# Performance work log

Hardware: AMD Instinct MI355X
Metric: run time of the kernel (lower is better)

The kernel has to match this reference:

```python
import jax, jax.numpy as jnp
import numpy as np

N_ATOMS = 32768
N_GRAPHS = 256
PER_GRAPH = 128
HIDDEN = 128
FILTERS = 128
NUM_GAUSS = 50
CUTOFF = 5.0
NUM_LAYERS = 3
OUT_CH = 1
BOX = 14.1
SLOPE = 0.015


def _lrelu(x):
    return jnp.where(x > 0, x, SLOPE * x)


def setup_inputs() -> dict:
    rng = np.random.default_rng(0)
    batch = np.repeat(np.arange(N_GRAPHS), PER_GRAPH).astype(np.int64)
    pos_np = rng.uniform(0.0, BOX, size=(N_ATOMS, 3)).astype(np.float32)
    # radius graph, built per-graph exactly like compute_radius_graph
    # (with global index offset so edges reference global node ids)
    edges = []
    for b in range(N_GRAPHS):
        pb = pos_np[b * PER_GRAPH:(b + 1) * PER_GRAPH]
        d = np.linalg.norm(pb[:, None, :] - pb[None, :, :], axis=-1)
        src, dst = np.where((d <= CUTOFF) & (d > 0))
        edges.append(np.stack([src, dst], axis=0) + b * PER_GRAPH)
    edge_index = np.concatenate(edges, axis=1).astype(np.int64)
    z = rng.integers(0, 100, size=(N_ATOMS,)).astype(np.int64)

    key = jax.random.key(0)
    ks = jax.random.split(key, 12)

    def xavier(k, shape):
        fan_in, fan_out = shape[-2], shape[-1]
        s = float(np.sqrt(6.0 / (fan_in + fan_out)))
        return jax.random.uniform(k, shape, jnp.float32, -s, s)

    L = NUM_LAYERS
    params = dict(
        emb=jax.random.normal(ks[0], (100, HIDDEN), jnp.float32),
        w_lin=xavier(ks[1], (L, HIDDEN, FILTERS)),
        mlp_w1=xavier(ks[2], (L, NUM_GAUSS, FILTERS)), mlp_b1=jnp.zeros((L, FILTERS), jnp.float32),
        mlp_w2=xavier(ks[3], (L, FILTERS, FILTERS)), mlp_b2=jnp.zeros((L, FILTERS), jnp.float32),
        mlp_w3=xavier(ks[4], (L, FILTERS, FILTERS)), mlp_b3=jnp.zeros((L, FILTERS), jnp.float32),
        lout_w=xavier(ks[5], (L, FILTERS, FILTERS)), lout_b=jnp.zeros((L, FILTERS), jnp.float32),
        v_w1=xavier(ks[6], (L, FILTERS, HIDDEN)), v_b1=jnp.zeros((L, HIDDEN), jnp.float32),
        v_w2=xavier(ks[7], (L, HIDDEN, HIDDEN)), v_b2=jnp.zeros((L, HIDDEN), jnp.float32),
        u_w1=xavier(ks[8], (HIDDEN, HIDDEN // 2)), u_b1=jnp.zeros((HIDDEN // 2,), jnp.float32),
        u_w2=xavier(ks[9], (HIDDEN // 2, OUT_CH)), u_b2=jnp.zeros((OUT_CH,), jnp.float32),
    )
    return dict(z=jnp.asarray(z), pos=jnp.asarray(pos_np), batch=jnp.asarray(batch),
                edge_index=jnp.asarray(edge_index), **params)


def reference(z, pos, batch, edge_index, emb, w_lin,
              mlp_w1, mlp_b1, mlp_w2, mlp_b2, mlp_w3, mlp_b3,
              lout_w, lout_b, v_w1, v_b1, v_w2, v_b2,
              u_w1, u_b1, u_w2, u_b2):
    row, col = edge_index[0], edge_index[1]          # row = j (source), col = i (target)
    dist = jnp.linalg.norm(pos[row] - pos[col], axis=-1)        # [E]
    offset = jnp.linspace(0.0, CUTOFF, NUM_GAUSS)
    coeff = -0.5 / (offset[1] - offset[0]) ** 2
    dist_emb = jnp.exp(coeff * (dist[:, None] - offset[None, :]) ** 2)   # [E, G]
    C = 0.5 * (jnp.cos(dist * jnp.pi / CUTOFF) + 1.0)                    # [E]

    v = emb[z]                                                           # [N, H]
    for l in range(NUM_LAYERS):
        # UpdateE: filter MLP on distance embedding, cosine cutoff envelope
        h = _lrelu(dist_emb @ mlp_w1[l] + mlp_b1[l])
        h = _lrelu(h @ mlp_w2[l] + mlp_b2[l])
        W = (h @ mlp_w3[l] + mlp_b3[l]) * C[:, None]                     # [E, F]
        e = (v @ w_lin[l])[row] * W                                      # gather + modulate
        e = (e @ lout_w[l] + lout_b[l]) + e                              # residual edge lin
        # UpdateV: scatter-add into target nodes, then 2-layer MLP residual
        agg = jax.ops.segment_sum(e, col, num_segments=N_ATOMS)         # [N, F]
        v = v + (_lrelu(agg @ v_w1[l] + v_b1[l]) @ v_w2[l] + v_b2[l])

    # UpdateU: node MLP then per-graph mean pooling
    u = _lrelu(v @ u_w1 + u_b1) @ u_w2 + u_b2                            # [N, out]
    sums = jax.ops.segment_sum(u, batch, num_segments=N_GRAPHS)
    cnt = jax.ops.segment_sum(jnp.ones((u.shape[0],), u.dtype), batch, num_segments=N_GRAPHS)
    return jnp.where(cnt[:, None] > 0, sums / jnp.maximum(cnt, 1.0)[:, None], 0.0)
```

## Files before the change

kernel.cpp:

```cpp
#include <hip/hip_runtime.h>

typedef float f4 __attribute__((ext_vector_type(4)));
typedef float f2 __attribute__((ext_vector_type(2)));
typedef float f32x4 __attribute__((ext_vector_type(4)));
typedef short bf16x8 __attribute__((ext_vector_type(8)));
typedef short sh4 __attribute__((ext_vector_type(4)));

#define G_TAB 2048
#define SWZ(row, b) ((b) ^ (((row) & 7) << 4))

__device__ __forceinline__ float lrelu(float x) { return x > 0.f ? x : 0.015f * x; }

__device__ __forceinline__ short f2bf(float x) {
  union { float f; unsigned u; } v; v.f = x;
  unsigned r = v.u + 0x7fff + ((v.u >> 16) & 1);
  return (short)(r >> 16);
}
__device__ __forceinline__ float bf2f(short h) {
  union { float f; unsigned u; } v; v.u = ((unsigned)(unsigned short)h) << 16;
  return v.f;
}

__device__ __forceinline__ void st_pair(short* Hi, short* Lo, int row, int k, f4 x) {
  sh4 hi, lo;
  #pragma unroll
  for (int c = 0; c < 4; c++) { hi[c] = f2bf(x[c]); lo[c] = f2bf(x[c] - bf2f(hi[c])); }
  int b = row * 256 + SWZ(row, (k >> 3) * 16) + (k & 7) * 2;
  *(sh4*)((char*)Hi + b) = hi;
  *(sh4*)((char*)Lo + b) = lo;
}
__device__ __forceinline__ void st_pair1(short* Hi, short* Lo, int row, int k, float x) {
  short hi = f2bf(x), lo = f2bf(x - bf2f(hi));
  int b = row * 256 + SWZ(row, (k >> 3) * 16) + (k & 7) * 2;
  *(short*)((char*)Hi + b) = hi;
  *(short*)((char*)Lo + b) = lo;
}

template<int NFC, int CH>
__device__ __forceinline__ void mm16(const short* Ahi, const short* Alo,
    const short* __restrict__ BhT, const short* __restrict__ BlT,
    int w, int l, f32x4* acc) {
  int lr = l & 15, lk = l >> 4;
  #pragma unroll
  for (int fc = 0; fc < NFC; fc++) acc[fc] = (f32x4)0.f;
  #pragma unroll
  for (int ch = 0; ch < CH; ch++) {
    int arow = w * 16 + lr;
    int ab = arow * 256 + SWZ(arow, ch * 64 + lk * 16);
    bf16x8 ah = *(const bf16x8*)((const char*)Ahi + ab);
    bf16x8 al = *(const bf16x8*)((const char*)Alo + ab);
    #pragma unroll
    for (int fc = 0; fc < NFC; fc++) {
      int bcol = fc * 16 + lr;
      int bb = bcol * 256 + SWZ(bcol, ch * 64 + lk * 16);
      bf16x8 bh = *(const bf16x8*)((const char*)BhT + bb);
      bf16x8 bl = *(const bf16x8*)((const char*)BlT + bb);
      acc[fc] = __builtin_amdgcn_mfma_f32_16x16x32_bf16(ah, bh, acc[fc], 0, 0, 0);
      acc[fc] = __builtin_amdgcn_mfma_f32_16x16x32_bf16(al, bh, acc[fc], 0, 0, 0);
      acc[fc] = __builtin_amdgcn_mfma_f32_16x16x32_bf16(ah, bl, acc[fc], 0, 0, 0);
    }
  }
}


__global__ __launch_bounds__(256) void gather_emb(const int* __restrict__ z,
    const float* __restrict__ emb, float* __restrict__ v, int nf4) {
  int i = blockIdx.x * 256 + threadIdx.x;
  if (i >= nf4) return;
  int a = i >> 5, s = i & 31;
  ((f4*)v)[i] = ((const f4*)emb)[z[a] * 32 + s];
}

__global__ __launch_bounds__(256) void edge_geom(const int* __restrict__ ei,
    const float* __restrict__ pos, float* __restrict__ edc, int E) {
  int e = blockIdx.x * 256 + threadIdx.x;
  if (e >= E) return;
  int r = ei[e], c = ei[E + e];
  float dx = pos[3*r] - pos[3*c];
  float dy = pos[3*r+1] - pos[3*c+1];
  float dz = pos[3*r+2] - pos[3*c+2];
  float d = sqrtf(dx*dx + dy*dy + dz*dz);
  edc[2*e] = d;
  edc[2*e+1] = 0.5f * (cosf(d * 0.6283185307179586f) + 1.0f);
}

__global__ __launch_bounds__(256) void make_starts(const int* __restrict__ row,
    int* __restrict__ starts, int E, int N) {
  int i = blockIdx.x * 256 + threadIdx.x;
  if (i > N) return;
  int lo = 0, hi = E;
  while (lo < hi) { int mid = (lo + hi) >> 1; if (row[mid] < i) lo = mid + 1; else hi = mid; }
  starts[i] = lo;
}

__global__ __launch_bounds__(256) void convert_wt(const float* __restrict__ w_lin,
    const float* __restrict__ vw2, const float* __restrict__ uw1,
    const float* __restrict__ mw1, const float* __restrict__ mw2,
    const float* __restrict__ mw3, const float* __restrict__ vw1,
    short* __restrict__ dhi, short* __restrict__ dlo) {
  int y = blockIdx.y;
  int i = blockIdx.x * 256 + threadIdx.x;
  int j = i >> 7, k = i & 127;
  int slot; float x;
  if (y < 3)       { slot = y;     x = w_lin[(size_t)y*16384 + k*128 + j]; }
  else if (y < 6)  { slot = 3 + y; x = vw2[(size_t)(y-3)*16384 + k*128 + j]; }
  else if (y == 6) { slot = 9;     x = (j < 64) ? uw1[k*64 + j] : 0.f; }
  else if (y < 10) { slot = 3 + y; x = mw2[(size_t)(y-7)*16384 + k*128 + j]; }
  else if (y < 13) { slot = 3 + y; x = mw3[(size_t)(y-10)*16384 + k*128 + j]; }
  else if (y < 16) { slot = 3 + y; x = (k < 50) ? mw1[(size_t)(y-13)*6400 + k*128 + j] : 0.f; }
  else             { slot = 3 + y; x = vw1[(size_t)(y-16)*16384 + k*128 + j]; }
  short hi = f2bf(x);
  int ob = j * 256 + (((k >> 3) * 16) ^ ((j & 7) << 4)) + (k & 7) * 2;
  char* bh = (char*)dhi + (size_t)slot * 32768;
  char* bl = (char*)dlo + (size_t)slot * 32768;
  *(short*)(bh + ob) = hi;
  *(short*)(bl + ob) = f2bf(x - bf2f(hi));
}

__global__ __launch_bounds__(128) void make_c1(const float* __restrict__ lball,
    const float* __restrict__ w1all, float* __restrict__ c1all) {
  int l = blockIdx.y;
  const float* lb = lball + (size_t)l * 128;
  const float* w1 = w1all + (size_t)l * 16384;
  int j = threadIdx.x;
  float s = 0.f;
  for (int k = 0; k < 128; k++) s += lb[k] * w1[k * 128 + j];
  c1all[l * 128 + j] = s;
}

__global__ __launch_bounds__(512) void prep_M(const float* __restrict__ loutw,
    short* __restrict__ whiT, short* __restrict__ wloT) {
  __shared__ __align__(16) short Ahi[16384];
  __shared__ __align__(16) short Alo[16384];
  int tid = threadIdx.x;
  int lay = blockIdx.x;
  int w = tid >> 6, l = tid & 63;
  int lr = l & 15, lk = l >> 4;
  int arow = w * 16 + (l >> 2), sub = l & 3;
  const f4* src = (const f4*)(loutw + (size_t)lay*16384 + (size_t)arow*128 + sub*32);
  #pragma unroll
  for (int q = 0; q < 8; q++) {
    f4 x = src[q];
    int kb = sub * 32 + q * 4;
    #pragma unroll
    for (int cc = 0; cc < 4; cc++) if (arow == kb + cc) x[cc] += 1.0f;
    st_pair(Ahi, Alo, arow, kb, x);
  }
  __syncthreads();
  f32x4 acc[8];
  mm16<8,4>(Ahi, Alo, whiT + (size_t)(19+lay)*16384, wloT + (size_t)(19+lay)*16384, w, l, acc);
  char* bh = (char*)whiT + (size_t)(3+lay) * 32768;
  char* bl = (char*)wloT + (size_t)(3+lay) * 32768;
  #pragma unroll
  for (int r = 0; r < 4; r++)
    #pragma unroll
    for (int fc = 0; fc < 8; fc++) {
      int row = w*16 + lk*4 + r, col = fc*16 + lr;
      float val = acc[fc][r];
      short hi = f2bf(val);
      int ob = col * 256 + (((row >> 3) * 16) ^ ((col & 7) << 4)) + (row & 7) * 2;
      *(short*)(bh + ob) = hi;
      *(short*)(bl + ob) = f2bf(val - bf2f(hi));
    }
}

__global__ __launch_bounds__(512) void table_mfma(
    const short* __restrict__ whiT, const short* __restrict__ wloT,
    const float* __restrict__ mb1, const float* __restrict__ mb2,
    const float* __restrict__ mb3, float* __restrict__ tables) {
  __shared__ __align__(16) short Ahi[16384];
  __shared__ __align__(16) short Alo[16384];
  __shared__ __align__(16) short Bhi[16384];
  __shared__ __align__(16) short Blo[16384];
  int tid = threadIdx.x;
  int lay = blockIdx.y;
  int p0 = blockIdx.x * 128;
  int w = tid >> 6, l = tid & 63;
  int lr = l & 15, lk = l >> 4;
  int prow = w * 16 + (l >> 2), sub = l & 3;
  const float delta = 5.0f / (G_TAB - 1);
  {
    float d = (p0 + prow) * delta;
    #pragma unroll
    for (int q = 0; q < 4; q++) {
      f4 x;
      #pragma unroll
      for (int cc = 0; cc < 4; cc++) {
        int k = sub * 16 + q * 4 + cc;
        float t = d - k * (5.0f / 49.0f);
        x[cc] = (k < 50) ? expf(-48.02f * t * t) : 0.f;
      }
      st_pair(Ahi, Alo, prow, sub * 16 + q * 4, x);
    }
  }
  __syncthreads();
  f32x4 acc[8];
  mm16<8,2>(Ahi, Alo, whiT + (size_t)(16+lay)*16384, wloT + (size_t)(16+lay)*16384, w, l, acc);
  #pragma unroll
  for (int r = 0; r < 4; r++)
    #pragma unroll
    for (int fc = 0; fc < 8; fc++)
      st_pair1(Bhi, Blo, w*16 + lk*4 + r, fc*16 + lr,
               lrelu(acc[fc][r] + mb1[lay*128 + fc*16 + lr]));
  __syncthreads();
  mm16<8,4>(Bhi, Blo, whiT + (size_t)(10+lay)*16384, wloT + (size_t)(10+lay)*16384, w, l, acc);
  #pragma unroll
  for (int r = 0; r < 4; r++)
    #pragma unroll
    for (int fc = 0; fc < 8; fc++)
      st_pair1(Ahi, Alo, w*16 + lk*4 + r, fc*16 + lr,
               lrelu(acc[fc][r] + mb2[lay*128 + fc*16 + lr]));
  __syncthreads();
  mm16<8,4>(Ahi, Alo, whiT + (size_t)(13+lay)*16384, wloT + (size_t)(13+lay)*16384, w, l, acc);
  float* tb = tables + (size_t)lay * G_TAB * 128;
  #pragma unroll
  for (int r = 0; r < 4; r++)
    #pragma unroll
    for (int fc = 0; fc < 8; fc++)
      tb[(size_t)(p0 + w*16 + lk*4 + r) * 128 + fc*16 + lr] =
          acc[fc][r] + mb3[lay*128 + fc*16 + lr];
}


template<int ACT, int ACC, int BIAS>
__global__ __launch_bounds__(256) void gemm128b(
    const float* __restrict__ A, const short* __restrict__ BhS,
    const short* __restrict__ BlS, const float* __restrict__ bias,
    const float* __restrict__ bias2, const float* __restrict__ rs,
    float* __restrict__ out) {
  __shared__ __align__(16) short Bhi[16384];
  __shared__ __align__(16) short Blo[16384];
  int tid = threadIdx.x;
  int p = blockIdx.x;
  size_t row0 = (size_t)(((p & 7) << 5) + (p >> 3)) * 128;
  #pragma unroll
  for (int s = 0; s < 8; s++) {
    ((bf16x8*)Bhi)[tid + 256*s] = ((const bf16x8*)BhS)[tid + 256*s];
    ((bf16x8*)Blo)[tid + 256*s] = ((const bf16x8*)BlS)[tid + 256*s];
  }
  __syncthreads();
  int w = tid >> 6, l = tid & 63, lr = l & 15, lk = l >> 4;
  #pragma unroll
  for (int half = 0; half < 2; half++) {
    int rbase = half * 64 + w * 16;
    const float* ap0 = A + (row0 + rbase + lr) * 128;
    bf16x8 ah[4], al[4];
    #pragma unroll
    for (int ch = 0; ch < 4; ch++) {
      const f4* ap = (const f4*)(ap0 + ch*32 + lk*8);
      f4 x0 = ap[0], x1 = ap[1];
      #pragma unroll
      for (int c = 0; c < 4; c++) {
        short h0 = f2bf(x0[c]);
        ah[ch][c] = h0; al[ch][c] = f2bf(x0[c] - bf2f(h0));
        short h1 = f2bf(x1[c]);
        ah[ch][c+4] = h1; al[ch][c+4] = f2bf(x1[c] - bf2f(h1));
      }
    }
    f32x4 acc[8];
    #pragma unroll
    for (int fc = 0; fc < 8; fc++) acc[fc] = (f32x4)0.f;
    #pragma unroll
    for (int ch = 0; ch < 4; ch++)
      #pragma unroll
      for (int fc = 0; fc < 8; fc++) {
        int bcol = fc*16 + lr;
        int bb = bcol*256 + SWZ(bcol, ch*64 + lk*16);
        bf16x8 bh = *(const bf16x8*)((const char*)Bhi + bb);
        bf16x8 bl = *(const bf16x8*)((const char*)Blo + bb);
        acc[fc] = __builtin_amdgcn_mfma_f32_16x16x32_bf16(ah[ch], bh, acc[fc], 0, 0, 0);
        acc[fc] = __builtin_amdgcn_mfma_f32_16x16x32_bf16(al[ch], bh, acc[fc], 0, 0, 0);
        acc[fc] = __builtin_amdgcn_mfma_f32_16x16x32_bf16(ah[ch], bl, acc[fc], 0, 0, 0);
      }
    #pragma unroll
    for (int r = 0; r < 4; r++) {
      size_t grow = row0 + rbase + lk*4 + r;
      float rsv = (BIAS == 3) ? rs[grow] : 0.f;
      #pragma unroll
      for (int fc = 0; fc < 8; fc++) {
        int col = fc*16 + lr;
        float val = acc[fc][r];
        if (BIAS == 1) val += bias[col];
        if (BIAS == 3) val += rsv * bias[col] + bias2[col];
        if (ACT) val = lrelu(val);
        float* op = &out[grow * 128 + col];
        if (ACC) val += *op;
        *op = val;
      }
    }
  }
}

__global__ __launch_bounds__(256) void edge_gather(
    const int* __restrict__ ei, const int* __restrict__ starts,
    const float* __restrict__ edc, const float* __restrict__ vlin,
    const float* __restrict__ table, float* __restrict__ S,
    float* __restrict__ deg, int E, int N) {
  int tid = threadIdx.x;
  int lane = tid & 31, grp = tid >> 5;
  int p = blockIdx.x;
  int o = ((p & 7) << 9) + (p >> 3);
  int a = o * 8 + grp;
  if (a >= N) return;
  int s = starts[a], e_end = starts[a + 1];
  int j0 = lane * 4;
  const float sc = (float)(G_TAB - 1) / 5.0f;
  f4 acc = (f4)0.f;
  int e = s;
  for (; e + 1 < e_end; e += 2) {
    int c0 = ei[E + e], c1 = ei[E + e + 1];
    f2 dc0 = *(const f2*)&edc[2 * e];
    f2 dc1 = *(const f2*)&edc[2 * e + 2];
    float u0 = dc0[0] * sc, u1 = dc1[0] * sc;
    int i0 = (int)u0; if (i0 > G_TAB - 2) i0 = G_TAB - 2;
    int i1 = (int)u1; if (i1 > G_TAB - 2) i1 = G_TAB - 2;
    float f0 = u0 - (float)i0, f1 = u1 - (float)i1;
    f4 t00 = *(const f4*)&table[(size_t)i0 * 128 + j0];
    f4 t01 = *(const f4*)&table[(size_t)i0 * 128 + 128 + j0];
    f4 vl0 = *(const f4*)&vlin[(size_t)c0 * 128 + j0];
    f4 t10 = *(const f4*)&table[(size_t)i1 * 128 + j0];
    f4 t11 = *(const f4*)&table[(size_t)i1 * 128 + 128 + j0];
    f4 vl1 = *(const f4*)&vlin[(size_t)c1 * 128 + j0];
    acc += vl0 * ((t00 + f0 * (t01 - t00)) * dc0[1]);
    acc += vl1 * ((t10 + f1 * (t11 - t10)) * dc1[1]);
  }
  if (e < e_end) {
    int c0 = ei[E + e];
    f2 dc0 = *(const f2*)&edc[2 * e];
    float u0 = dc0[0] * sc;
    int i0 = (int)u0; if (i0 > G_TAB - 2) i0 = G_TAB - 2;
    float f0 = u0 - (float)i0;
    f4 t00 = *(const f4*)&table[(size_t)i0 * 128 + j0];
    f4 t01 = *(const f4*)&table[(size_t)i0 * 128 + 128 + j0];
    f4 vl0 = *(const f4*)&vlin[(size_t)c0 * 128 + j0];
    acc += vl0 * ((t00 + f0 * (t01 - t00)) * dc0[1]);
  }
  *(f4*)&S[(size_t)a * 128 + j0] = acc;
  if (lane == 0) deg[a] = (float)(e_end - s);
}

__global__ __launch_bounds__(256) void readout_b(const float* __restrict__ v,
    const short* __restrict__ Bh9, const short* __restrict__ Bl9,
    const float* __restrict__ ub1, const float* __restrict__ uw2,
    float* __restrict__ y) {
  __shared__ __align__(16) short Bh[8192];
  __shared__ __align__(16) short Bl[8192];
  int tid = threadIdx.x;
  int p = blockIdx.x;
  size_t row0 = (size_t)(((p & 7) << 5) + (p >> 3)) * 128;
  #pragma unroll
  for (int s = 0; s < 4; s++) {
    ((bf16x8*)Bh)[tid + 256*s] = ((const bf16x8*)Bh9)[tid + 256*s];
    ((bf16x8*)Bl)[tid + 256*s] = ((const bf16x8*)Bl9)[tid + 256*s];
  }
  __syncthreads();
  int w = tid >> 6, l = tid & 63, lr = l & 15, lk = l >> 4;
  #pragma unroll
  for (int half = 0; half < 2; half++) {
    int rbase = half * 64 + w * 16;
    const float* ap0 = v + (row0 + rbase + lr) * 128;
    bf16x8 ah[4], al[4];
    #pragma unroll
    for (int ch = 0; ch < 4; ch++) {
      const f4* ap = (const f4*)(ap0 + ch*32 + lk*8);
      f4 x0 = ap[0], x1 = ap[1];
      #pragma unroll
      for (int c = 0; c < 4; c++) {
        short h0 = f2bf(x0[c]);
        ah[ch][c] = h0; al[ch][c] = f2bf(x0[c] - bf2f(h0));
        short h1 = f2bf(x1[c]);
        ah[ch][c+4] = h1; al[ch][c+4] = f2bf(x1[c] - bf2f(h1));
      }
    }
    f32x4 acc[4];
    #pragma unroll
    for (int fc = 0; fc < 4; fc++) acc[fc] = (f32x4)0.f;
    #pragma unroll
    for (int ch = 0; ch < 4; ch++)
      #pragma unroll
      for (int fc = 0; fc < 4; fc++) {
        int bcol = fc*16 + lr;
        int bb = bcol*256 + SWZ(bcol, ch*64 + lk*16);
        bf16x8 bh = *(const bf16x8*)((const char*)Bh + bb);
        bf16x8 bl = *(const bf16x8*)((const char*)Bl + bb);
        acc[fc] = __builtin_amdgcn_mfma_f32_16x16x32_bf16(ah[ch], bh, acc[fc], 0, 0, 0);
        acc[fc] = __builtin_amdgcn_mfma_f32_16x16x32_bf16(al[ch], bh, acc[fc], 0, 0, 0);
        acc[fc] = __builtin_amdgcn_mfma_f32_16x16x32_bf16(ah[ch], bl, acc[fc], 0, 0, 0);
      }
    #pragma unroll
    for (int r = 0; r < 4; r++) {
      float sv = 0.f;
      #pragma unroll
      for (int fc = 0; fc < 4; fc++) {
        int col = fc*16 + lr;
        sv += lrelu(acc[fc][r] + ub1[col]) * uw2[col];
      }
      sv += __shfl_xor(sv, 1); sv += __shfl_xor(sv, 2);
      sv += __shfl_xor(sv, 4); sv += __shfl_xor(sv, 8);
      if (lr == 0) y[row0 + rbase + lk*4 + r] = sv;
    }
  }
}

__global__ __launch_bounds__(256) void graph_mean(const float* __restrict__ y,
    const float* __restrict__ ub2, float* __restrict__ out) {
  __shared__ float red[256];
  int tid = threadIdx.x;
  red[tid] = y[blockIdx.x * 256 + tid];
  __syncthreads();
  for (int s = 64; s > 0; s >>= 1) {
    if ((tid & 127) < s) red[tid] += red[tid + s];
    __syncthreads();
  }
  if ((tid & 127) == 0)
    out[blockIdx.x * 2 + (tid >> 7)] = red[tid] * (1.0f / 128.0f) + ub2[0];
}

extern "C" void kernel_launch(void* const* d_in, const int* in_sizes, int n_in,
                              void* d_out, int out_size, void* d_ws, size_t ws_size,
                              hipStream_t stream) {
  const int*   z     = (const int*)d_in[0];
  const float* pos   = (const float*)d_in[1];
  const int*   ei    = (const int*)d_in[3];
  const float* emb   = (const float*)d_in[4];
  const float* w_lin = (const float*)d_in[5];
  const float* mw1   = (const float*)d_in[6];
  const float* mb1   = (const float*)d_in[7];
  const float* mw2   = (const float*)d_in[8];
  const float* mb2   = (const float*)d_in[9];
  const float* mw3   = (const float*)d_in[10];
  const float* mb3   = (const float*)d_in[11];
  const float* loutw = (const float*)d_in[12];
  const float* loutb = (const float*)d_in[13];
  const float* vw1   = (const float*)d_in[14];
  const float* vb1   = (const float*)d_in[15];
  const float* vw2   = (const float*)d_in[16];
  const float* vb2   = (const float*)d_in[17];
  const float* uw1   = (const float*)d_in[18];
  const float* ub1   = (const float*)d_in[19];
  const float* uw2   = (const float*)d_in[20];
  const float* ub2   = (const float*)d_in[21];
  int N = in_sizes[0];
  int E = in_sizes[3] / 2;
  float* out = (float*)d_out;

  size_t off = 0;
  auto alloc = [&](size_t bytes) -> void* {
    void* p = (char*)d_ws + off;
    off += (bytes + 255) & ~(size_t)255;
    return p;
  };
  float* v      = (float*)alloc((size_t)N * 128 * 4);
  float* bufA   = (float*)alloc((size_t)N * 128 * 4);
  float* bufB   = (float*)alloc((size_t)N * 128 * 4);
  float* bufC   = (float*)alloc((size_t)N * 128 * 4);
  float* tables = (float*)alloc((size_t)3 * G_TAB * 128 * 4);
  short* whiT   = (short*)alloc((size_t)22 * 16384 * 2);
  short* wloT   = (short*)alloc((size_t)22 * 16384 * 2);
  float* c1s    = (float*)alloc(3 * 128 * 4);
  float* deg    = (float*)alloc((size_t)N * 4);
  float* edc    = (float*)alloc((size_t)E * 8);
  int*   starts = (int*)alloc((size_t)(N + 1) * 4);
  float* y      = (float*)alloc((size_t)N * 4);

  gather_emb<<<(N * 32 + 255) / 256, 256, 0, stream>>>(z, emb, v, N * 32);
  edge_geom<<<(E + 255) / 256, 256, 0, stream>>>(ei, pos, edc, E);
  make_starts<<<(N + 256) / 256, 256, 0, stream>>>(ei, starts, E, N);
  convert_wt<<<dim3(64, 19), 256, 0, stream>>>(w_lin, vw2, uw1, mw1, mw2, mw3, vw1,
                                               whiT, wloT);
  prep_M<<<3, 512, 0, stream>>>(loutw, whiT, wloT);
  make_c1<<<dim3(1, 3), 128, 0, stream>>>(loutb, vw1, c1s);
  table_mfma<<<dim3(G_TAB / 128, 3), 512, 0, stream>>>(whiT, wloT, mb1, mb2, mb3, tables);

  for (int l = 0; l < 3; l++) {
    gemm128b<0, 0, 0><<<N / 128, 256, 0, stream>>>(
        v, whiT + (size_t)l * 16384, wloT + (size_t)l * 16384,
        nullptr, nullptr, nullptr, bufA);
    edge_gather<<<(N + 7) / 8, 256, 0, stream>>>(ei, starts, edc, bufA,
                                                 tables + (size_t)l * G_TAB * 128,
                                                 bufB, deg, E, N);
    gemm128b<1, 0, 3><<<N / 128, 256, 0, stream>>>(
        bufB, whiT + (size_t)(3 + l) * 16384, wloT + (size_t)(3 + l) * 16384,
        c1s + (size_t)l * 128, vb1 + (size_t)l * 128, deg, bufC);
    gemm128b<0, 1, 1><<<N / 128, 256, 0, stream>>>(
        bufC, whiT + (size_t)(6 + l) * 16384, wloT + (size_t)(6 + l) * 16384,
        vb2 + (size_t)l * 128, nullptr, nullptr, v);
  }
  readout_b<<<N / 128, 256, 0, stream>>>(v, whiT + (size_t)9 * 16384,
                                         wloT + (size_t)9 * 16384, ub1, uw2, y);
  graph_mean<<<N / 256, 256, 0, stream>>>(y, ub2, out);
}
```

Measured before the change: 306.3 us.

## Store filter tables in bf16, read low weights from global, unroll gather by four

The precomputed distance filter tables are now written and read as bf16 rather than fp32, which halves table traffic in the edge gather. The edge gather loop is unrolled to four edges so more independent loads are in flight. The GEMM and readout kernels no longer stage the low-part weights in LDS and read them straight from global memory, halving their shared memory use. The convert_wt index mapping is also swapped so global reads coalesce. Rounding the table to bf16 adds approximation error to the filter values.

Measured after the change: 308.7 us. Within noise of the previous version (+0.8%).

```diff
diff --git a/kernel.cpp b/kernel.cpp
--- a/kernel.cpp
+++ b/kernel.cpp
@@ -5,6 +5,7 @@
 typedef float f32x4 __attribute__((ext_vector_type(4)));
 typedef short bf16x8 __attribute__((ext_vector_type(8)));
 typedef short sh4 __attribute__((ext_vector_type(4)));
+typedef unsigned short us4 __attribute__((ext_vector_type(4)));
 
 #define G_TAB 2048
 #define SWZ(row, b) ((b) ^ (((row) & 7) << 4))
@@ -18,6 +19,10 @@
 }
 __device__ __forceinline__ float bf2f(short h) {
   union { float f; unsigned u; } v; v.u = ((unsigned)(unsigned short)h) << 16;
+  return v.f;
+}
+__device__ __forceinline__ float bf2fu(unsigned short h) {
+  union { float f; unsigned u; } v; v.u = ((unsigned)h) << 16;
   return v.f;
 }
 
@@ -100,7 +105,7 @@
     short* __restrict__ dhi, short* __restrict__ dlo) {
   int y = blockIdx.y;
   int i = blockIdx.x * 256 + threadIdx.x;
-  int j = i >> 7, k = i & 127;
+  int k = i >> 7, j = i & 127;
   int slot; float x;
   if (y < 3)       { slot = y;     x = w_lin[(size_t)y*16384 + k*128 + j]; }
   else if (y < 6)  { slot = 3 + y; x = vw2[(size_t)(y-3)*16384 + k*128 + j]; }
@@ -167,7 +172,7 @@
 __global__ __launch_bounds__(512) void table_mfma(
     const short* __restrict__ whiT, const short* __restrict__ wloT,
     const float* __restrict__ mb1, const float* __restrict__ mb2,
-    const float* __restrict__ mb3, float* __restrict__ tables) {
+    const float* __restrict__ mb3, unsigned short* __restrict__ tables) {
   __shared__ __align__(16) short Ahi[16384];
   __shared__ __align__(16) short Alo[16384];
   __shared__ __align__(16) short Bhi[16384];
@@ -212,13 +217,13 @@
                lrelu(acc[fc][r] + mb2[lay*128 + fc*16 + lr]));
   __syncthreads();
   mm16<8,4>(Ahi, Alo, whiT + (size_t)(13+lay)*16384, wloT + (size_t)(13+lay)*16384, w, l, acc);
-  float* tb = tables + (size_t)lay * G_TAB * 128;
+  unsigned short* tb = tables + (size_t)lay * G_TAB * 128;
   #pragma unroll
   for (int r = 0; r < 4; r++)
     #pragma unroll
     for (int fc = 0; fc < 8; fc++)
       tb[(size_t)(p0 + w*16 + lk*4 + r) * 128 + fc*16 + lr] =
-          acc[fc][r] + mb3[lay*128 + fc*16 + lr];
+          (unsigned short)f2bf(acc[fc][r] + mb3[lay*128 + fc*16 + lr]);
 }
 
 
@@ -229,17 +234,15 @@
     const float* __restrict__ bias2, const float* __restrict__ rs,
     float* __restrict__ out) {
   __shared__ __align__(16) short Bhi[16384];
-  __shared__ __align__(16) short Blo[16384];
   int tid = threadIdx.x;
   int p = blockIdx.x;
   size_t row0 = (size_t)(((p & 7) << 5) + (p >> 3)) * 128;
   #pragma unroll
-  for (int s = 0; s < 8; s++) {
+  for (int s = 0; s < 8; s++)
     ((bf16x8*)Bhi)[tid + 256*s] = ((const bf16x8*)BhS)[tid + 256*s];
-    ((bf16x8*)Blo)[tid + 256*s] = ((const bf16x8*)BlS)[tid + 256*s];
-  }
   __syncthreads();
   int w = tid >> 6, l = tid & 63, lr = l & 15, lk = l >> 4;
+  const char* BlB = (const char*)BlS;
   #pragma unroll
   for (int half = 0; half < 2; half++) {
     int rbase = half * 64 + w * 16;
@@ -267,7 +270,7 @@
         int bcol = fc*16 + lr;
         int bb = bcol*256 + SWZ(bcol, ch*64 + lk*16);
         bf16x8 bh = *(const bf16x8*)((const char*)Bhi + bb);
-        bf16x8 bl = *(const bf16x8*)((const char*)Blo + bb);
+        bf16x8 bl = *(const bf16x8*)(BlB + bb);
         acc[fc] = __builtin_amdgcn_mfma_f32_16x16x32_bf16(ah[ch], bh, acc[fc], 0, 0, 0);
         acc[fc] = __builtin_amdgcn_mfma_f32_16x16x32_bf16(al[ch], bh, acc[fc], 0, 0, 0);
         acc[fc] = __builtin_amdgcn_mfma_f32_16x16x32_bf16(ah[ch], bl, acc[fc], 0, 0, 0);
@@ -294,7 +297,7 @@
 __global__ __launch_bounds__(256) void edge_gather(
     const int* __restrict__ ei, const int* __restrict__ starts,
     const float* __restrict__ edc, const float* __restrict__ vlin,
-    const float* __restrict__ table, float* __restrict__ S,
+    const unsigned short* __restrict__ tb, float* __restrict__ S,
     float* __restrict__ deg, int E, int N) {
   int tid = threadIdx.x;
   int lane = tid & 31, grp = tid >> 5;
@@ -302,41 +305,49 @@
   int o = ((p & 7) << 9) + (p >> 3);
   int a = o * 8 + grp;
   if (a >= N) return;
-  int s = starts[a], e_end = starts[a + 1];
+  int s = starts[a], ee = starts[a + 1];
   int j0 = lane * 4;
   const float sc = (float)(G_TAB - 1) / 5.0f;
   f4 acc = (f4)0.f;
   int e = s;
-  for (; e + 1 < e_end; e += 2) {
-    int c0 = ei[E + e], c1 = ei[E + e + 1];
-    f2 dc0 = *(const f2*)&edc[2 * e];
-    f2 dc1 = *(const f2*)&edc[2 * e + 2];
-    float u0 = dc0[0] * sc, u1 = dc1[0] * sc;
-    int i0 = (int)u0; if (i0 > G_TAB - 2) i0 = G_TAB - 2;
-    int i1 = (int)u1; if (i1 > G_TAB - 2) i1 = G_TAB - 2;
-    float f0 = u0 - (float)i0, f1 = u1 - (float)i1;
-    f4 t00 = *(const f4*)&table[(size_t)i0 * 128 + j0];
-    f4 t01 = *(const f4*)&table[(size_t)i0 * 128 + 128 + j0];
-    f4 vl0 = *(const f4*)&vlin[(size_t)c0 * 128 + j0];
-    f4 t10 = *(const f4*)&table[(size_t)i1 * 128 + j0];
-    f4 t11 = *(const f4*)&table[(size_t)i1 * 128 + 128 + j0];
-    f4 vl1 = *(const f4*)&vlin[(size_t)c1 * 128 + j0];
-    acc += vl0 * ((t00 + f0 * (t01 - t00)) * dc0[1]);
-    acc += vl1 * ((t10 + f1 * (t11 - t10)) * dc1[1]);
-  }
-  if (e < e_end) {
+  for (; e + 3 < ee; e += 4) {
+    int cc[4]; f2 dd[4];
+    #pragma unroll
+    for (int q = 0; q < 4; q++) { cc[q] = ei[E + e + q]; dd[q] = *(const f2*)&edc[2*(e+q)]; }
+    f4 vl[4]; us4 t0[4], t1[4]; float ff[4];
+    #pragma unroll
+    for (int q = 0; q < 4; q++) {
+      float u = dd[q][0] * sc;
+      int i0 = (int)u; if (i0 > G_TAB - 2) i0 = G_TAB - 2;
+      ff[q] = u - (float)i0;
+      t0[q] = *(const us4*)&tb[(size_t)i0 * 128 + j0];
+      t1[q] = *(const us4*)&tb[(size_t)i0 * 128 + 128 + j0];
+      vl[q] = *(const f4*)&vlin[(size_t)cc[q] * 128 + j0];
+    }
+    #pragma unroll
+    for (int q = 0; q < 4; q++) {
+      f4 T0, T1;
+      #pragma unroll
+      for (int c4 = 0; c4 < 4; c4++) { T0[c4] = bf2fu(t0[q][c4]); T1[c4] = bf2fu(t1[q][c4]); }
+      acc += vl[q] * ((T0 + ff[q] * (T1 - T0)) * dd[q][1]);
+    }
+  }
+  for (; e < ee; e++) {
     int c0 = ei[E + e];
     f2 dc0 = *(const f2*)&edc[2 * e];
-    float u0 = dc0[0] * sc;
-    int i0 = (int)u0; if (i0 > G_TAB - 2) i0 = G_TAB - 2;
-    float f0 = u0 - (float)i0;
-    f4 t00 = *(const f4*)&table[(size_t)i0 * 128 + j0];
-    f4 t01 = *(const f4*)&table[(size_t)i0 * 128 + 128 + j0];
-    f4 vl0 = *(const f4*)&vlin[(size_t)c0 * 128 + j0];
-    acc += vl0 * ((t00 + f0 * (t01 - t00)) * dc0[1]);
+    float u = dc0[0] * sc;
+    int i0 = (int)u; if (i0 > G_TAB - 2) i0 = G_TAB - 2;
+    float f = u - (float)i0;
+    us4 t0 = *(const us4*)&tb[(size_t)i0 * 128 + j0];
+    us4 t1 = *(const us4*)&tb[(size_t)i0 * 128 + 128 + j0];
+    f4 vl = *(const f4*)&vlin[(size_t)c0 * 128 + j0];
+    f4 T0, T1;
+    #pragma unroll
+    for (int c4 = 0; c4 < 4; c4++) { T0[c4] = bf2fu(t0[c4]); T1[c4] = bf2fu(t1[c4]); }
+    acc += vl * ((T0 + f * (T1 - T0)) * dc0[1]);
   }
   *(f4*)&S[(size_t)a * 128 + j0] = acc;
-  if (lane == 0) deg[a] = (float)(e_end - s);
+  if (lane == 0) deg[a] = (float)(ee - s);
 }
 
 __global__ __launch_bounds__(256) void readout_b(const float* __restrict__ v,
@@ -344,17 +355,15 @@
     const float* __restrict__ ub1, const float* __restrict__ uw2,
     float* __restrict__ y) {
   __shared__ __align__(16) short Bh[8192];
-  __shared__ __align__(16) short Bl[8192];
   int tid = threadIdx.x;
   int p = blockIdx.x;
   size_t row0 = (size_t)(((p & 7) << 5) + (p >> 3)) * 128;
   #pragma unroll
-  for (int s = 0; s < 4; s++) {
+  for (int s = 0; s < 4; s++)
     ((bf16x8*)Bh)[tid + 256*s] = ((const bf16x8*)Bh9)[tid + 256*s];
-    ((bf16x8*)Bl)[tid + 256*s] = ((const bf16x8*)Bl9)[tid + 256*s];
-  }
   __syncthreads();
   int w = tid >> 6, l = tid & 63, lr = l & 15, lk = l >> 4;
+  const char* BlB = (const char*)Bl9;
   #pragma unroll
   for (int half = 0; half < 2; half++) {
     int rbase = half * 64 + w * 16;
@@ -382,7 +391,7 @@
         int bcol = fc*16 + lr;
         int bb = bcol*256 + SWZ(bcol, ch*64 + lk*16);
         bf16x8 bh = *(const bf16x8*)((const char*)Bh + bb);
-        bf16x8 bl = *(const bf16x8*)((const char*)Bl + bb);
+        bf16x8 bl = *(const bf16x8*)(BlB + bb);
         acc[fc] = __builtin_amdgcn_mfma_f32_16x16x32_bf16(ah[ch], bh, acc[fc], 0, 0, 0);
         acc[fc] = __builtin_amdgcn_mfma_f32_16x16x32_bf16(al[ch], bh, acc[fc], 0, 0, 0);
         acc[fc] = __builtin_amdgcn_mfma_f32_16x16x32_bf16(ah[ch], bl, acc[fc], 0, 0, 0);
@@ -454,7 +463,7 @@
   float* bufA   = (float*)alloc((size_t)N * 128 * 4);
   float* bufB   = (float*)alloc((size_t)N * 128 * 4);
   float* bufC   = (float*)alloc((size_t)N * 128 * 4);
-  float* tables = (float*)alloc((size_t)3 * G_TAB * 128 * 4);
+  unsigned short* tables = (unsigned short*)alloc((size_t)3 * G_TAB * 128 * 2);
   short* whiT   = (short*)alloc((size_t)22 * 16384 * 2);
   short* wloT   = (short*)alloc((size_t)22 * 16384 * 2);
   float* c1s    = (float*)alloc(3 * 128 * 4);
```
